# Kernel tuning notes

Hardware: AMD Instinct MI355X
Metric: run time of the kernel (lower is better)

The kernel has to match this reference:

```python
import jax, jax.numpy as jnp
import numpy as np

B, T, C = 2, 4096, 2048
N = 64
H = C // N
D_W, D_A, D_MV, D_G = 96, 96, 64, 256
LN_EPS = 0.00064


def setup_inputs() -> dict:
    key = jax.random.key(0)
    ks = jax.random.split(key, 32)
    rn = lambda k, shape, s=1.0: jax.random.normal(k, shape, jnp.float32) * s
    inp = {}
    inp["x"] = rn(ks[0], (B, T, C))
    inp["v_first"] = rn(ks[1], (B, T, C))
    # token-shift mixing coefficients (in (0,1) like 1 - ddd**p)
    for i, name in enumerate(["x_r", "x_w", "x_k", "x_v", "x_a", "x_g"]):
        inp[name] = jax.random.uniform(ks[2 + i], (1, 1, C), jnp.float32)
    # decay LoRA: w0 in roughly [-6, -0.5]
    inp["w0"] = jax.random.uniform(ks[8], (1, 1, C), jnp.float32, -6.0, -0.5)
    inp["w1"] = rn(ks[9], (C, D_W), 0.05)
    inp["w2"] = rn(ks[10], (D_W, C), 0.05)
    # in-context-learning-rate (a) LoRA
    inp["a0"] = rn(ks[11], (1, 1, C), 0.3) - 0.19
    inp["a1"] = rn(ks[12], (C, D_A), 0.05)
    inp["a2"] = rn(ks[13], (D_A, C), 0.05)
    # value-mix LoRA (layer_id > 0)
    inp["v0"] = rn(ks[14], (1, 1, C), 0.2) + 0.73
    inp["v1"] = rn(ks[15], (C, D_MV), 0.05)
    inp["v2"] = rn(ks[16], (D_MV, C), 0.05)
    # gate LoRA
    inp["g1"] = rn(ks[17], (C, D_G), 0.05)
    inp["g2"] = rn(ks[18], (D_G, C), 0.05)
    inp["k_k"] = rn(ks[19], (1, 1, C), 0.05) + 0.71
    inp["k_a"] = rn(ks[20], (1, 1, C), 0.02) + 1.02
    inp["r_k"] = rn(ks[21], (H, N), 0.02) - 0.04
    sc = 0.5 / C ** 0.5
    inp["W_r"] = jax.random.uniform(ks[22], (C, C), jnp.float32, -sc, sc)
    inp["W_k"] = jax.random.uniform(ks[23], (C, C), jnp.float32, -0.1 * sc, 0.1 * sc)
    inp["W_v"] = jax.random.uniform(ks[24], (C, C), jnp.float32, -sc, sc)
    inp["W_o"] = rn(ks[25], (C, C), 0.02)
    inp["ln_w"] = jnp.ones((C,), jnp.float32)
    inp["ln_b"] = jnp.zeros((C,), jnp.float32)
    return inp


def _wkv7(r, wdec, k, v, a, b):
    # r,wdec,k,v,a,b: [B,T,C]; per-head delta-rule scan, state S: [B,H,Nv,Nk]
    def heads(t):
        return t.reshape(B, T, H, N).transpose(1, 0, 2, 3)  # [T,B,H,N]

    def step(S, ins):
        r_t, w_t, k_t, v_t, a_t, b_t = ins  # each [B,H,N]
        sa = jnp.einsum('bhvk,bhk->bhv', S, a_t)
        S = (S * w_t[:, :, None, :]
             + sa[..., None] * b_t[:, :, None, :]
             + v_t[..., None] * k_t[:, :, None, :])
        y_t = jnp.einsum('bhvk,bhk->bhv', S, r_t)
        return S, y_t

    S0 = jnp.zeros((B, H, N, N), r.dtype)
    _, ys = jax.lax.scan(step, S0, (heads(r), heads(wdec), heads(k), heads(v), heads(a), heads(b)))
    return ys.transpose(1, 0, 2, 3).reshape(B, T, C)


def reference(x, v_first, x_r, x_w, x_k, x_v, x_a, x_g,
              w0, w1, w2, a0, a1, a2, v0, v1, v2, g1, g2,
              k_k, k_a, r_k, W_r, W_k, W_v, W_o, ln_w, ln_b):
    # token shift: prepend zero row, drop last
    xx = jnp.concatenate([jnp.zeros_like(x[:, :1]), x[:, :-1]], axis=1) - x
    xr = x + xx * x_r
    xw = x + xx * x_w
    xk = x + xx * x_k
    xv = x + xx * x_v
    xa = x + xx * x_a
    xg = x + xx * x_g
    r = xr @ W_r.T
    k = xk @ W_k.T
    v = xv @ W_v.T
    w = -jax.nn.softplus(-(w0 + jnp.tanh(xw @ w1) @ w2)) - 0.5
    # layer_id > 0: mix with first-layer value
    v = v + (v_first - v) * jax.nn.sigmoid(v0 + xv @ v1 @ v2)
    a = jax.nn.sigmoid(a0 + xa @ a1 @ a2)
    g = jax.nn.sigmoid(xg @ g1) @ g2
    kk = k * k_k
    kkh = kk.reshape(B, T, H, N)
    kkh = kkh / jnp.maximum(jnp.linalg.norm(kkh, axis=-1, keepdims=True), 1e-12)
    kk = kkh.reshape(B, T, C)
    k = k * (1.0 + (a - 1.0) * k_a)
    wdec = jnp.exp(-jnp.exp(w))  # RWKV7 decay parameterization
    y = _wkv7(r, wdec, k, v, -kk, kk * a)
    # GroupNorm(H groups) over channels per token
    yh = y.reshape(B, T, H, N)
    mu = yh.mean(-1, keepdims=True)
    var = yh.var(-1, keepdims=True)
    y = ((yh - mu) / jnp.sqrt(var + LN_EPS)).reshape(B, T, C) * ln_w + ln_b
    # bonus term
    rh, kh, vh = (t.reshape(B, T, H, N) for t in (r, k, v))
    bonus = ((rh * kh * r_k).sum(-1, keepdims=True) * vh).reshape(B, T, C)
    y = y + bonus
    return (y * g) @ W_o.T
```

## Files before the change

kernel.cpp:

```cpp
#include <hip/hip_runtime.h>
#include <hip/hip_bf16.h>
#include <stdint.h>
#include <math.h>

#define DEV __device__ __forceinline__

typedef __hip_bfloat16 bf16;
typedef __attribute__((ext_vector_type(8))) __bf16 bf16x8;
typedef __attribute__((ext_vector_type(4))) float f32x4;
typedef __attribute__((ext_vector_type(2))) float f32x2;

static constexpr int B_ = 2;
static constexpr int T_ = 4096;
static constexpr int C_ = 2048;
static constexpr int H_ = 32;

DEV void gld_lds16(const void* g, void* l) {
  __builtin_amdgcn_global_load_lds((const __attribute__((address_space(1))) void*)g,
                                   (__attribute__((address_space(3))) void*)l, 16, 0, 0);
}
DEV float bfbits2f(unsigned short u) {
  unsigned int x = ((unsigned int)u) << 16;
  return __builtin_bit_cast(float, x);
}
DEV unsigned short f2bfbits(float f) { bf16 h = __float2bfloat16(f); return __builtin_bit_cast(unsigned short, h); }
DEV void store_bf16x4(bf16* p, f32x4 v) {
  ushort4 u;
  u.x = f2bfbits(v.x); u.y = f2bfbits(v.y); u.z = f2bfbits(v.z); u.w = f2bfbits(v.w);
  *reinterpret_cast<ushort4*>(p) = u;
}
DEV float wsum64(float v) {
#pragma unroll
  for (int m = 32; m > 0; m >>= 1) v += __shfl_xor(v, m, 64);
  return v;
}
template<int CTRL>
DEV float dpp_add(float v) {
  int x = __builtin_bit_cast(int, v);
  int y = __builtin_amdgcn_update_dpp(0, x, CTRL, 0xf, 0xf, false);
  return v + __builtin_bit_cast(float, y);
}
DEV float red16(float v) {
  v = dpp_add<0xB1>(v);
  v = dpp_add<0x4E>(v);
  v = dpp_add<0x124>(v);
  v = dpp_add<0x128>(v);
  return v;
}
DEV f32x4 cvt4(uint2 u) {
  f32x4 o;
  o.x = __builtin_bit_cast(float, u.x << 16);
  o.y = __builtin_bit_cast(float, u.x & 0xFFFF0000u);
  o.z = __builtin_bit_cast(float, u.y << 16);
  o.w = __builtin_bit_cast(float, u.y & 0xFFFF0000u);
  return o;
}

template<int MODE>
__global__ __launch_bounds__(256)
void gemm_bt(const bf16* __restrict__ A, const bf16* __restrict__ Bm,
             void* __restrict__ Cout, const float* __restrict__ ep,
             int N, int K, int T4)
{
  __shared__ bf16 lA[128 * 64];
  __shared__ bf16 lB[128 * 64];
  const int tid  = threadIdx.x;
  const int wave = tid >> 6;
  const int lane = tid & 63;
  const long brow = (long)blockIdx.x * 128;
  const long bcol = (long)blockIdx.y * 128;
  const int wr = wave >> 1, wc = wave & 1;

  f32x4 acc[4][4];
#pragma unroll
  for (int m = 0; m < 4; ++m)
#pragma unroll
    for (int n = 0; n < 4; ++n)
      acc[m][n] = f32x4{0.f, 0.f, 0.f, 0.f};

  const bf16* pa = A  + (size_t)(brow + wave * 32 + (lane >> 3)) * K + (lane & 7) * 8;
  const bf16* pb = Bm + (size_t)(bcol + wave * 32 + (lane >> 3)) * K + (lane & 7) * 8;

  for (int k0 = 0; k0 < K; k0 += 64) {
#pragma unroll
    for (int i = 0; i < 4; ++i) gld_lds16(pa + (size_t)i * 8 * K, &lA[(wave * 4 + i) * 512]);
#pragma unroll
    for (int i = 0; i < 4; ++i) gld_lds16(pb + (size_t)i * 8 * K, &lB[(wave * 4 + i) * 512]);
    pa += 64; pb += 64;
    __syncthreads();
#pragma unroll
    for (int kk = 0; kk < 2; ++kk) {
      bf16x8 af[4], bfv[4];
#pragma unroll
      for (int m = 0; m < 4; ++m)
        af[m] = *(const bf16x8*)&lA[(wr * 64 + m * 16 + (lane & 15)) * 64 + kk * 32 + (lane >> 4) * 8];
#pragma unroll
      for (int n = 0; n < 4; ++n)
        bfv[n] = *(const bf16x8*)&lB[(wc * 64 + n * 16 + (lane & 15)) * 64 + kk * 32 + (lane >> 4) * 8];
#pragma unroll
      for (int m = 0; m < 4; ++m)
#pragma unroll
        for (int n = 0; n < 4; ++n)
          acc[m][n] = __builtin_amdgcn_mfma_f32_16x16x32_bf16(af[m], bfv[n], acc[m][n], 0, 0, 0);
    }
    __syncthreads();
  }

  const int cr = (lane >> 4) * 4;
  const int cc = lane & 15;
#pragma unroll
  for (int m = 0; m < 4; ++m) {
#pragma unroll
    for (int n = 0; n < 4; ++n) {
#pragma unroll
      for (int j = 0; j < 4; ++j) {
        long gm = brow + wr * 64 + m * 16 + cr + j;
        long gn = bcol + wc * 64 + n * 16 + cc;
        float val = acc[m][n][j];
        if constexpr (MODE == 0) {
          ((float*)Cout)[gm * N + gn] = val;
        } else if constexpr (MODE == 2) {
          ((bf16*)Cout)[gm * N + gn] = __float2bfloat16(val);
        } else if constexpr (MODE == 3) {
          ((bf16*)Cout)[gm * N + gn] = __float2bfloat16(tanhf(val));
        } else if constexpr (MODE == 4) {
          ((bf16*)Cout)[gm * N + gn] = __float2bfloat16(1.f / (1.f + expf(-val)));
        } else if constexpr (MODE == 7) {
          long b = gm / T4, t = gm % T4;
          ((bf16*)Cout)[((b * (N >> 6) + (gn >> 6)) * T4 + t) * 64 + (gn & 63)] = __float2bfloat16(val);
        } else if constexpr (MODE == 8) {
          float u = ep[gn] + val;
          float w = -log1pf(expf(-u)) - 0.5f;
          float wd = expf(-expf(w));
          long b = gm / T4, t = gm % T4;
          ((float*)Cout)[((b * (N >> 6) + (gn >> 6)) * T4 + t) * 64 + (gn & 63)] = wd;
        } else if constexpr (MODE == 9) {
          float sg = 1.f / (1.f + expf(-(ep[gn] + val)));
          long b = gm / T4, t = gm % T4;
          ((bf16*)Cout)[((b * (N >> 6) + (gn >> 6)) * T4 + t) * 64 + (gn & 63)] = __float2bfloat16(sg);
        }
      }
    }
  }
}

__global__ __launch_bounds__(256)
void mix1(const float* __restrict__ x, const float* __restrict__ coef,
          bf16* __restrict__ out)
{
  size_t e = ((size_t)blockIdx.x * 256 + threadIdx.x) * 4;
  int c = (int)(e & (C_ - 1));
  size_t m = e >> 11;
  f32x4 xc = *(const f32x4*)(x + e);
  f32x4 xp;
  if ((m & (T_ - 1)) == 0) xp = f32x4{0.f, 0.f, 0.f, 0.f};
  else                     xp = *(const f32x4*)(x + e - C_);
  f32x4 cf = *(const f32x4*)(coef + c);
  store_bf16x4(out + e, xc + (xp - xc) * cf);
}

__global__ __launch_bounds__(256)
void cvt1(const float* __restrict__ s, bf16* __restrict__ d)
{
  size_t e = ((size_t)blockIdx.x * 256 + threadIdx.x) * 4;
  store_bf16x4(d + e, *(const f32x4*)(s + e));
}

struct TPJob { const float* s; bf16* d; int R, Cs, NP, RP; };
struct TP8 { TPJob j[8]; };
__global__ __launch_bounds__(256)
void tpad(TP8 jobs)
{
  TPJob J = jobs.j[blockIdx.y];
  int i = blockIdx.x * 256 + threadIdx.x;
  int tot = J.NP * J.RP;
  if (i >= tot) return;
  int n = i / J.RP, r = i - n * J.RP;
  float v = (n < J.Cs && r < J.R) ? J.s[(size_t)r * J.Cs + n] : 0.f;
  J.d[i] = __float2bfloat16(v);
}

__global__ __launch_bounds__(256)
void prescan2(const bf16* __restrict__ r16, bf16* __restrict__ k16,
              bf16* __restrict__ v16, bf16* __restrict__ ab,
              bf16* __restrict__ vn16,
              const float* __restrict__ vfirst, const float* __restrict__ kkc,
              const float* __restrict__ kac, const float* __restrict__ rk,
              float* __restrict__ sbonus)
{
  const int wid = threadIdx.x >> 6;
  const int lane = threadIdx.x & 63;
  const long id = (long)blockIdx.x * 4 + wid;
  const long bh = id >> 12;
  const long t = id & (T_ - 1);
  const long b = bh >> 5, h = bh & (H_ - 1);
  const long mrow = b * T_ + t;
  const int c = (int)(h * 64 + lane);
  const size_t tp = (size_t)id * 64 + lane;
  float k  = __bfloat162float(k16[tp]);
  float v  = __bfloat162float(v16[tp]);
  float r  = __bfloat162float(r16[tp]);
  float a  = __bfloat162float(ab[tp]);
  float vs = __bfloat162float(vn16[tp]);
  float vf = vfirst[mrow * C_ + c];
  float kkv = k * kkc[c];
  float ssum = wsum64(kkv * kkv);
  float kkn = kkv / fmaxf(sqrtf(ssum), 1e-12f);
  float kn = k * (1.f + (a - 1.f) * kac[c]);
  float vn = v + (vf - v) * vs;
  k16[tp] = __float2bfloat16(kn);
  v16[tp] = __float2bfloat16(vn);
  ab[tp]  = __float2bfloat16(kkn * a);
  vn16[tp] = __float2bfloat16(kkn);
  float bs = wsum64(r * kn * rk[c]);
  if (lane == 0) sbonus[id] = bs;
}

struct SS {
  uint2 r0, r1, k0, k1, n0, n1, b0, b1;
  f32x4 w0, w1;
  unsigned short v0, v1;
};
DEV SS ldss(const uint2* pr, const uint2* pk, const uint2* pn, const uint2* pb,
            const f32x4* pw, const unsigned short* pv, int ss, int kq, int row)
{
  SS s;
  int i0 = ss * 32 + kq, i1 = i0 + 16;
  s.r0 = pr[i0]; s.r1 = pr[i1];
  s.k0 = pk[i0]; s.k1 = pk[i1];
  s.n0 = pn[i0]; s.n1 = pn[i1];
  s.b0 = pb[i0]; s.b1 = pb[i1];
  s.w0 = pw[i0]; s.w1 = pw[i1];
  int j0 = ss * 128 + row, j1 = j0 + 64;
  s.v0 = pv[j0]; s.v1 = pv[j1];
  return s;
}
DEV float dostep(f32x4& S, uint2 ru, uint2 ku, uint2 nu, uint2 bu,
                 f32x4 W, unsigned short vus)
{
  f32x4 R = cvt4(ru), K = cvt4(ku), N = cvt4(nu), Bv = cvt4(bu);
  float vt = bfbits2f(vus);
  f32x2 acc = S.xy * N.xy;
  acc = __builtin_elementwise_fma(S.zw, N.zw, acc);
  float sa = red16(acc.x + acc.y);
  float nsa = -sa;
  f32x2 ns2 = f32x2{nsa, nsa}, vt2 = f32x2{vt, vt};
  S.xy = __builtin_elementwise_fma(vt2, K.xy,
           __builtin_elementwise_fma(ns2, Bv.xy, S.xy * W.xy));
  S.zw = __builtin_elementwise_fma(vt2, K.zw,
           __builtin_elementwise_fma(ns2, Bv.zw, S.zw * W.zw));
  f32x2 yq = S.xy * R.xy;
  yq = __builtin_elementwise_fma(S.zw, R.zw, yq);
  return red16(yq.x + yq.y);
}
DEV void consume(f32x4& S, const SS& s, bf16* py, int t, int kq)
{
  float y0 = dostep(S, s.r0, s.k0, s.n0, s.b0, s.w0, s.v0);
  if (kq == 0) py[(size_t)t * 64] = __float2bfloat16(y0);
  float y1 = dostep(S, s.r1, s.k1, s.n1, s.b1, s.w1, s.v1);
  if (kq == 0) py[(size_t)(t + 1) * 64] = __float2bfloat16(y1);
}
__global__ __launch_bounds__(256, 1)
void wkv_scan5(const bf16* __restrict__ r16, const float* __restrict__ w32,
               const bf16* __restrict__ k16, const bf16* __restrict__ v16,
               const bf16* __restrict__ n16, const bf16* __restrict__ b16,
               bf16* __restrict__ y16)
{
  const int bh = blockIdx.x & 63;
  const int quarter = blockIdx.x >> 6;
  const int wv = threadIdx.x >> 6;
  const int lane = threadIdx.x & 63;
  const int vl = lane >> 4;
  const int kq = lane & 15;
  const int row = quarter * 16 + wv * 4 + vl;
  const size_t eb = (size_t)bh * (T_ * 64);
  const uint2* pr = (const uint2*)(r16 + eb);
  const uint2* pk = (const uint2*)(k16 + eb);
  const uint2* pn = (const uint2*)(n16 + eb);
  const uint2* pb = (const uint2*)(b16 + eb);
  const f32x4* pw = (const f32x4*)(w32 + eb);
  const unsigned short* pv = (const unsigned short*)(v16 + eb);
  bf16* py = y16 + eb + row;

  f32x4 S = f32x4{0.f, 0.f, 0.f, 0.f};
  const int NS = T_ / 2;

  SS s0 = ldss(pr, pk, pn, pb, pw, pv, 0, kq, row);
  SS s1 = ldss(pr, pk, pn, pb, pw, pv, 1, kq, row);
  SS s2 = ldss(pr, pk, pn, pb, pw, pv, 2, kq, row);
  SS s3 = ldss(pr, pk, pn, pb, pw, pv, 3, kq, row);

  for (int ss = 0; ss < NS; ss += 4) {
    int n0 = ss + 4 < NS ? ss + 4 : NS - 1;
    int n1 = ss + 5 < NS ? ss + 5 : NS - 1;
    int n2 = ss + 6 < NS ? ss + 6 : NS - 1;
    int n3 = ss + 7 < NS ? ss + 7 : NS - 1;
    SS p0 = ldss(pr, pk, pn, pb, pw, pv, n0, kq, row);
    consume(S, s0, py, 2 * ss, kq);
    SS p1 = ldss(pr, pk, pn, pb, pw, pv, n1, kq, row);
    consume(S, s1, py, 2 * ss + 2, kq);
    SS p2 = ldss(pr, pk, pn, pb, pw, pv, n2, kq, row);
    consume(S, s2, py, 2 * ss + 4, kq);
    SS p3 = ldss(pr, pk, pn, pb, pw, pv, n3, kq, row);
    consume(S, s3, py, 2 * ss + 6, kq);
    s0 = p0; s1 = p1; s2 = p2; s3 = p3;
  }
}

__global__ __launch_bounds__(256)
void postk2(const bf16* __restrict__ y16, const bf16* __restrict__ v16,
            const float* __restrict__ sbonus, const bf16* __restrict__ g16,
            const float* __restrict__ lnw, const float* __restrict__ lnb,
            bf16* __restrict__ opre)
{
  const int wid = threadIdx.x >> 6;
  const int lane = threadIdx.x & 63;
  const long id = (long)blockIdx.x * 4 + wid;
  const long bh = id >> 12;
  const long t = id & (T_ - 1);
  const long b = bh >> 5, h = bh & (H_ - 1);
  const long mrow = b * T_ + t;
  const int c = (int)(h * 64 + lane);
  const size_t tp = (size_t)id * 64 + lane;
  float y = __bfloat162float(y16[tp]);
  float mu = wsum64(y) * (1.f / 64.f);
  float d = y - mu;
  float var = wsum64(d * d) * (1.f / 64.f);
  float yn = d * rsqrtf(var + 0.00064f) * lnw[c] + lnb[c];
  float outv = (yn + sbonus[id] * __bfloat162float(v16[tp]))
               * __bfloat162float(g16[mrow * C_ + c]);
  opre[mrow * C_ + c] = __float2bfloat16(outv);
}

extern "C" void kernel_launch(void* const* d_in, const int* in_sizes, int n_in,
                              void* d_out, int out_size, void* d_ws, size_t ws_size,
                              hipStream_t stream)
{
  const float* x    = (const float*)d_in[0];
  const float* vfst = (const float*)d_in[1];
  const float* x_r  = (const float*)d_in[2];
  const float* x_w  = (const float*)d_in[3];
  const float* x_k  = (const float*)d_in[4];
  const float* x_v  = (const float*)d_in[5];
  const float* x_a  = (const float*)d_in[6];
  const float* x_g  = (const float*)d_in[7];
  const float* w0   = (const float*)d_in[8];
  const float* w1   = (const float*)d_in[9];
  const float* w2   = (const float*)d_in[10];
  const float* a0   = (const float*)d_in[11];
  const float* a1   = (const float*)d_in[12];
  const float* a2   = (const float*)d_in[13];
  const float* v0   = (const float*)d_in[14];
  const float* v1   = (const float*)d_in[15];
  const float* v2   = (const float*)d_in[16];
  const float* g1   = (const float*)d_in[17];
  const float* g2   = (const float*)d_in[18];
  const float* k_k  = (const float*)d_in[19];
  const float* k_a  = (const float*)d_in[20];
  const float* r_k  = (const float*)d_in[21];
  const float* W_r  = (const float*)d_in[22];
  const float* W_k  = (const float*)d_in[23];
  const float* W_v  = (const float*)d_in[24];
  const float* W_o  = (const float*)d_in[25];
  const float* lnw  = (const float*)d_in[26];
  const float* lnb  = (const float*)d_in[27];

  const size_t MB = 1048576ULL;
  const size_t HK = 524288ULL;
  if (ws_size < 248 * MB) return;

  char* ws = (char*)d_ws;
  bf16* r16  = (bf16*)(ws + 0 * MB);
  bf16* k16  = (bf16*)(ws + 32 * MB);
  bf16* v16  = (bf16*)(ws + 64 * MB);
  float* w32 = (float*)(ws + 96 * MB);
  bf16* opre = (bf16*)(ws + 96 * MB);
  bf16* asig = (bf16*)(ws + 160 * MB);
  bf16* vsig = (bf16*)(ws + 192 * MB);
  bf16* w1t = (bf16*)(ws + 224 * MB);
  bf16* a1t = (bf16*)(ws + 224 * MB + HK);
  bf16* v1t = (bf16*)(ws + 225 * MB);
  bf16* g1t = (bf16*)(ws + 225 * MB + HK);
  bf16* w2t = (bf16*)(ws + 226 * MB + HK);
  bf16* a2t = (bf16*)(ws + 227 * MB);
  bf16* v2t = (bf16*)(ws + 227 * MB + HK);
  bf16* g2t = (bf16*)(ws + 228 * MB);
  bf16* h_w = (bf16*)(ws + 229 * MB);
  bf16* h_a = (bf16*)(ws + 231 * MB);
  bf16* h_v = (bf16*)(ws + 233 * MB);
  bf16* h_g = (bf16*)(ws + 235 * MB);
  float* sb = (float*)(ws + 239 * MB);
  bf16* WB  = (bf16*)(ws + 240 * MB);
  bf16* g16 = (bf16*)d_out;
  bf16* MIX = (bf16*)((char*)d_out + 32 * MB);
  bf16* y16 = (bf16*)((char*)d_out + 32 * MB);

  TP8 jobs;
  jobs.j[0] = TPJob{ w1, w1t, 2048,   96,  128, 2048 };
  jobs.j[1] = TPJob{ a1, a1t, 2048,   96,  128, 2048 };
  jobs.j[2] = TPJob{ v1, v1t, 2048,   64,  128, 2048 };
  jobs.j[3] = TPJob{ g1, g1t, 2048,  256,  256, 2048 };
  jobs.j[4] = TPJob{ w2, w2t,   96, 2048, 2048,  128 };
  jobs.j[5] = TPJob{ a2, a2t,   96, 2048, 2048,  128 };
  jobs.j[6] = TPJob{ v2, v2t,   64, 2048, 2048,  128 };
  jobs.j[7] = TPJob{ g2, g2t,  256, 2048, 2048,  256 };
  tpad<<<dim3(2048, 8), 256, 0, stream>>>(jobs);

  mix1<<<dim3(16384), 256, 0, stream>>>(x, x_w, MIX);
  gemm_bt<3><<<dim3(64, 1), 256, 0, stream>>>(MIX, w1t, h_w, nullptr, 128, 2048, 0);
  mix1<<<dim3(16384), 256, 0, stream>>>(x, x_a, MIX);
  gemm_bt<2><<<dim3(64, 1), 256, 0, stream>>>(MIX, a1t, h_a, nullptr, 128, 2048, 0);
  mix1<<<dim3(16384), 256, 0, stream>>>(x, x_v, MIX);
  gemm_bt<2><<<dim3(64, 1), 256, 0, stream>>>(MIX, v1t, h_v, nullptr, 128, 2048, 0);
  mix1<<<dim3(16384), 256, 0, stream>>>(x, x_g, MIX);
  gemm_bt<4><<<dim3(64, 2), 256, 0, stream>>>(MIX, g1t, h_g, nullptr, 256, 2048, 0);

  gemm_bt<8><<<dim3(64, 16), 256, 0, stream>>>(h_w, w2t, w32, w0, 2048, 128, T_);
  gemm_bt<9><<<dim3(64, 16), 256, 0, stream>>>(h_a, a2t, asig, a0, 2048, 128, T_);
  gemm_bt<9><<<dim3(64, 16), 256, 0, stream>>>(h_v, v2t, vsig, v0, 2048, 128, T_);
  gemm_bt<2><<<dim3(64, 16), 256, 0, stream>>>(h_g, g2t, g16, nullptr, 2048, 256, 0);

  cvt1<<<dim3(4096), 256, 0, stream>>>(W_r, WB);
  mix1<<<dim3(16384), 256, 0, stream>>>(x, x_r, MIX);
  gemm_bt<7><<<dim3(64, 16), 256, 0, stream>>>(MIX, WB, r16, nullptr, 2048, 2048, T_);
  cvt1<<<dim3(4096), 256, 0, stream>>>(W_k, WB);
  mix1<<<dim3(16384), 256, 0, stream>>>(x, x_k, MIX);
  gemm_bt<7><<<dim3(64, 16), 256, 0, stream>>>(MIX, WB, k16, nullptr, 2048, 2048, T_);
  cvt1<<<dim3(4096), 256, 0, stream>>>(W_v, WB);
  mix1<<<dim3(16384), 256, 0, stream>>>(x, x_v, MIX);
  gemm_bt<7><<<dim3(64, 16), 256, 0, stream>>>(MIX, WB, v16, nullptr, 2048, 2048, T_);

  prescan2<<<dim3(65536), 256, 0, stream>>>(r16, k16, v16, asig, vsig,
                                            vfst, k_k, k_a, r_k, sb);
  wkv_scan5<<<dim3(256), 256, 0, stream>>>(r16, w32, k16, v16, vsig, asig, y16);
  postk2<<<dim3(65536), 256, 0, stream>>>(y16, v16, sb, g16, lnw, lnb, opre);

  cvt1<<<dim3(4096), 256, 0, stream>>>(W_o, WB);
  gemm_bt<0><<<dim3(64, 16), 256, 0, stream>>>(opre, WB, (float*)d_out, nullptr, 2048, 2048, 0);
}
```

Baseline: 1.952 ms.

## Split WKV scan state across 32 lanes per row and double block count

The recurrent WKV scan now gives each state row to 32 lanes holding 2 state elements each, instead of 16 lanes holding 4. The grid doubles from 256 to 512 blocks and launch bounds allow two blocks per CU, which should put more waves on the latency-bound serial scan. The price is an extra cross-row shuffle in every reduction and more total load instructions for the same data.

Result: slower. 2.136 ms (+9.4%).

```diff
diff --git a/kernel.cpp b/kernel.cpp
--- a/kernel.cpp
+++ b/kernel.cpp
@@ -18,10 +18,6 @@
 DEV void gld_lds16(const void* g, void* l) {
   __builtin_amdgcn_global_load_lds((const __attribute__((address_space(1))) void*)g,
                                    (__attribute__((address_space(3))) void*)l, 16, 0, 0);
-}
-DEV float bfbits2f(unsigned short u) {
-  unsigned int x = ((unsigned int)u) << 16;
-  return __builtin_bit_cast(float, x);
 }
 DEV unsigned short f2bfbits(float f) { bf16 h = __float2bfloat16(f); return __builtin_bit_cast(unsigned short, h); }
 DEV void store_bf16x4(bf16* p, f32x4 v) {
@@ -29,6 +25,10 @@
   u.x = f2bfbits(v.x); u.y = f2bfbits(v.y); u.z = f2bfbits(v.z); u.w = f2bfbits(v.w);
   *reinterpret_cast<ushort4*>(p) = u;
 }
+DEV float bfbits2f(unsigned short u) {
+  unsigned int x = ((unsigned int)u) << 16;
+  return __builtin_bit_cast(float, x);
+}
 DEV float wsum64(float v) {
 #pragma unroll
   for (int m = 32; m > 0; m >>= 1) v += __shfl_xor(v, m, 64);
@@ -40,19 +40,18 @@
   int y = __builtin_amdgcn_update_dpp(0, x, CTRL, 0xf, 0xf, false);
   return v + __builtin_bit_cast(float, y);
 }
-DEV float red16(float v) {
+DEV float red32(float v) {
   v = dpp_add<0xB1>(v);
   v = dpp_add<0x4E>(v);
   v = dpp_add<0x124>(v);
   v = dpp_add<0x128>(v);
+  v += __shfl_xor(v, 16, 64);
   return v;
 }
-DEV f32x4 cvt4(uint2 u) {
-  f32x4 o;
-  o.x = __builtin_bit_cast(float, u.x << 16);
-  o.y = __builtin_bit_cast(float, u.x & 0xFFFF0000u);
-  o.z = __builtin_bit_cast(float, u.y << 16);
-  o.w = __builtin_bit_cast(float, u.y & 0xFFFF0000u);
+DEV f32x2 cvt2(unsigned int u) {
+  f32x2 o;
+  o.x = __builtin_bit_cast(float, u << 16);
+  o.y = __builtin_bit_cast(float, u & 0xFFFF0000u);
   return o;
 }
 
@@ -216,93 +215,90 @@
   if (lane == 0) sbonus[id] = bs;
 }
 
-struct SS {
-  uint2 r0, r1, k0, k1, n0, n1, b0, b1;
-  f32x4 w0, w1;
+struct SS2 {
+  unsigned int r0, r1, k0, k1, n0, n1, b0, b1;
+  f32x2 w0, w1;
   unsigned short v0, v1;
 };
-DEV SS ldss(const uint2* pr, const uint2* pk, const uint2* pn, const uint2* pb,
-            const f32x4* pw, const unsigned short* pv, int ss, int kq, int row)
-{
-  SS s;
-  int i0 = ss * 32 + kq, i1 = i0 + 16;
+DEV SS2 ldss2(const unsigned int* pr, const unsigned int* pk,
+              const unsigned int* pn, const unsigned int* pb,
+              const f32x2* pw, const unsigned short* pv, int ss, int kq, int row)
+{
+  SS2 s;
+  int i0 = ss * 64 + kq, i1 = i0 + 32;
   s.r0 = pr[i0]; s.r1 = pr[i1];
   s.k0 = pk[i0]; s.k1 = pk[i1];
   s.n0 = pn[i0]; s.n1 = pn[i1];
   s.b0 = pb[i0]; s.b1 = pb[i1];
   s.w0 = pw[i0]; s.w1 = pw[i1];
-  int j0 = ss * 128 + row, j1 = j0 + 64;
-  s.v0 = pv[j0]; s.v1 = pv[j1];
+  int j0 = ss * 128 + row;
+  s.v0 = pv[j0]; s.v1 = pv[j0 + 64];
   return s;
 }
-DEV float dostep(f32x4& S, uint2 ru, uint2 ku, uint2 nu, uint2 bu,
-                 f32x4 W, unsigned short vus)
-{
-  f32x4 R = cvt4(ru), K = cvt4(ku), N = cvt4(nu), Bv = cvt4(bu);
+DEV float dostep2(f32x2& S, unsigned int ru, unsigned int ku, unsigned int nu,
+                  unsigned int bu, f32x2 W, unsigned short vus)
+{
+  f32x2 R = cvt2(ru), K = cvt2(ku), N = cvt2(nu), Bv = cvt2(bu);
   float vt = bfbits2f(vus);
-  f32x2 acc = S.xy * N.xy;
-  acc = __builtin_elementwise_fma(S.zw, N.zw, acc);
-  float sa = red16(acc.x + acc.y);
+  f32x2 t = S * N;
+  float sa = red32(t.x + t.y);
   float nsa = -sa;
   f32x2 ns2 = f32x2{nsa, nsa}, vt2 = f32x2{vt, vt};
-  S.xy = __builtin_elementwise_fma(vt2, K.xy,
-           __builtin_elementwise_fma(ns2, Bv.xy, S.xy * W.xy));
-  S.zw = __builtin_elementwise_fma(vt2, K.zw,
-           __builtin_elementwise_fma(ns2, Bv.zw, S.zw * W.zw));
-  f32x2 yq = S.xy * R.xy;
-  yq = __builtin_elementwise_fma(S.zw, R.zw, yq);
-  return red16(yq.x + yq.y);
-}
-DEV void consume(f32x4& S, const SS& s, bf16* py, int t, int kq)
-{
-  float y0 = dostep(S, s.r0, s.k0, s.n0, s.b0, s.w0, s.v0);
+  S = __builtin_elementwise_fma(vt2, K,
+        __builtin_elementwise_fma(ns2, Bv, S * W));
+  f32x2 yq = S * R;
+  return red32(yq.x + yq.y);
+}
+DEV void consume2(f32x2& S, const SS2& s, bf16* py, int t, int kq)
+{
+  float y0 = dostep2(S, s.r0, s.k0, s.n0, s.b0, s.w0, s.v0);
   if (kq == 0) py[(size_t)t * 64] = __float2bfloat16(y0);
-  float y1 = dostep(S, s.r1, s.k1, s.n1, s.b1, s.w1, s.v1);
+  float y1 = dostep2(S, s.r1, s.k1, s.n1, s.b1, s.w1, s.v1);
   if (kq == 0) py[(size_t)(t + 1) * 64] = __float2bfloat16(y1);
 }
-__global__ __launch_bounds__(256, 1)
-void wkv_scan5(const bf16* __restrict__ r16, const float* __restrict__ w32,
+__global__ __launch_bounds__(256, 2)
+void wkv_scan6(const bf16* __restrict__ r16, const float* __restrict__ w32,
                const bf16* __restrict__ k16, const bf16* __restrict__ v16,
                const bf16* __restrict__ n16, const bf16* __restrict__ b16,
                bf16* __restrict__ y16)
 {
   const int bh = blockIdx.x & 63;
-  const int quarter = blockIdx.x >> 6;
+  const int g = blockIdx.x >> 6;
   const int wv = threadIdx.x >> 6;
   const int lane = threadIdx.x & 63;
-  const int vl = lane >> 4;
-  const int kq = lane & 15;
-  const int row = quarter * 16 + wv * 4 + vl;
+  const int vl = lane >> 5;
+  const int kq = lane & 31;
+  const int row = g * 8 + wv * 2 + vl;
   const size_t eb = (size_t)bh * (T_ * 64);
-  const uint2* pr = (const uint2*)(r16 + eb);
-  const uint2* pk = (const uint2*)(k16 + eb);
-  const uint2* pn = (const uint2*)(n16 + eb);
-  const uint2* pb = (const uint2*)(b16 + eb);
-  const f32x4* pw = (const f32x4*)(w32 + eb);
+  const unsigned int* pr = (const unsigned int*)(r16 + eb);
+  const unsigned int* pk = (const unsigned int*)(k16 + eb);
+  const unsigned int* pn = (const unsigned int*)(n16 + eb);
+  const unsigned int* pb = (const unsigned int*)(b16 + eb);
+  const f32x2* pw = (const f32x2*)(w32 + eb);
   const unsigned short* pv = (const unsigned short*)(v16 + eb);
   bf16* py = y16 + eb + row;
 
-  f32x4 S = f32x4{0.f, 0.f, 0.f, 0.f};
+  f32x2 S = f32x2{0.f, 0.f};
   const int NS = T_ / 2;
 
-  SS s0 = ldss(pr, pk, pn, pb, pw, pv, 0, kq, row);
-  SS s1 = ldss(pr, pk, pn, pb, pw, pv, 1, kq, row);
-  SS s2 = ldss(pr, pk, pn, pb, pw, pv, 2, kq, row);
-  SS s3 = ldss(pr, pk, pn, pb, pw, pv, 3, kq, row);
+  SS2 s0 = ldss2(pr, pk, pn, pb, pw, pv, 0, kq, row);
+  SS2 s1 = ldss2(pr, pk, pn, pb, pw, pv, 1, kq, row);
+  SS2 s2 = ldss2(pr, pk, pn, pb, pw, pv, 2, kq, row);
+  SS2 s3 = ldss2(pr, pk, pn, pb, pw, pv, 3, kq, row);
 
   for (int ss = 0; ss < NS; ss += 4) {
     int n0 = ss + 4 < NS ? ss + 4 : NS - 1;
     int n1 = ss + 5 < NS ? ss + 5 : NS - 1;
     int n2 = ss + 6 < NS ? ss + 6 : NS - 1;
     int n3 = ss + 7 < NS ? ss + 7 : NS - 1;
-    SS p0 = ldss(pr, pk, pn, pb, pw, pv, n0, kq, row);
-    consume(S, s0, py, 2 * ss, kq);
-    SS p1 = ldss(pr, pk, pn, pb, pw, pv, n1, kq, row);
-    consume(S, s1, py, 2 * ss + 2, kq);
-    SS p2 = ldss(pr, pk, pn, pb, pw, pv, n2, kq, row);
-    consume(S, s2, py, 2 * ss + 4, kq);
-    SS p3 = ldss(pr, pk, pn, pb, pw, pv, n3, kq, row);
-    consume(S, s3, py, 2 * ss + 6, kq);
+    SS2 p0 = ldss2(pr, pk, pn, pb, pw, pv, n0, kq, row);
+    consume2(S, s0, py, 2 * ss, kq);
+    SS2 p1 = ldss2(pr, pk, pn, pb, pw, pv, n1, kq, row);
+    consume2(S, s1, py, 2 * ss + 2, kq);
+    SS2 p2 = ldss2(pr, pk, pn, pb, pw, pv, n2, kq, row);
+    consume2(S, s2, py, 2 * ss + 4, kq);
+    SS2 p3 = ldss2(pr, pk, pn, pb, pw, pv, n3, kq, row);
+    consume2(S, s3, py, 2 * ss + 6, kq);
     s0 = p0; s1 = p1; s2 = p2; s3 = p3;
   }
 }
@@ -432,7 +428,7 @@
 
   prescan2<<<dim3(65536), 256, 0, stream>>>(r16, k16, v16, asig, vsig,
                                             vfst, k_k, k_a, r_k, sb);
-  wkv_scan5<<<dim3(256), 256, 0, stream>>>(r16, w32, k16, v16, vsig, asig, y16);
+  wkv_scan6<<<dim3(512), 256, 0, stream>>>(r16, w32, k16, v16, vsig, asig, y16);
   postk2<<<dim3(65536), 256, 0, stream>>>(y16, v16, sb, g16, lnw, lnb, opre);
 
   cvt1<<<dim3(4096), 256, 0, stream>>>(W_o, WB);
```

## Batch LoRA GEMMs into multi-job launches, fuse token-shift mixes and weight conversion

Applied to the files above, without the earlier changes.

The four LoRA token-shift mixes are computed in one kernel that reads x once and writes four bf16 buffers. The eight small LoRA GEMMs are grouped into two multi-job launches so their blocks run concurrently instead of as tiny serial grids. Weight conversion is fused with each R/K/V mix into one launch. The scan loop gets sched_barriers to pin load/compute interleaving. The epilogue mode becomes a runtime switch, which costs a little per-store branching, and the new mix buffers reuse workspace regions that are later overwritten.

Result: slower. 2.130 ms (+9.1%).

```diff
diff --git a/kernel.cpp b/kernel.cpp
--- a/kernel.cpp
+++ b/kernel.cpp
@@ -18,16 +18,16 @@
 DEV void gld_lds16(const void* g, void* l) {
   __builtin_amdgcn_global_load_lds((const __attribute__((address_space(1))) void*)g,
                                    (__attribute__((address_space(3))) void*)l, 16, 0, 0);
-}
-DEV float bfbits2f(unsigned short u) {
-  unsigned int x = ((unsigned int)u) << 16;
-  return __builtin_bit_cast(float, x);
 }
 DEV unsigned short f2bfbits(float f) { bf16 h = __float2bfloat16(f); return __builtin_bit_cast(unsigned short, h); }
 DEV void store_bf16x4(bf16* p, f32x4 v) {
   ushort4 u;
   u.x = f2bfbits(v.x); u.y = f2bfbits(v.y); u.z = f2bfbits(v.z); u.w = f2bfbits(v.w);
   *reinterpret_cast<ushort4*>(p) = u;
+}
+DEV float bfbits2f(unsigned short u) {
+  unsigned int x = ((unsigned int)u) << 16;
+  return __builtin_bit_cast(float, x);
 }
 DEV float wsum64(float v) {
 #pragma unroll
@@ -56,19 +56,14 @@
   return o;
 }
 
-template<int MODE>
-__global__ __launch_bounds__(256)
-void gemm_bt(const bf16* __restrict__ A, const bf16* __restrict__ Bm,
-             void* __restrict__ Cout, const float* __restrict__ ep,
-             int N, int K, int T4)
-{
-  __shared__ bf16 lA[128 * 64];
-  __shared__ bf16 lB[128 * 64];
+DEV void gemm_body(const bf16* __restrict__ A, const bf16* __restrict__ Bm,
+                   void* __restrict__ Cout, const float* __restrict__ ep,
+                   int N, int K, long brow, long bcol, int mode,
+                   bf16* lA, bf16* lB)
+{
   const int tid  = threadIdx.x;
   const int wave = tid >> 6;
   const int lane = tid & 63;
-  const long brow = (long)blockIdx.x * 128;
-  const long bcol = (long)blockIdx.y * 128;
   const int wr = wave >> 1, wc = wave & 1;
 
   f32x4 acc[4][4];
@@ -117,46 +112,96 @@
         long gm = brow + wr * 64 + m * 16 + cr + j;
         long gn = bcol + wc * 64 + n * 16 + cc;
         float val = acc[m][n][j];
-        if constexpr (MODE == 0) {
-          ((float*)Cout)[gm * N + gn] = val;
-        } else if constexpr (MODE == 2) {
-          ((bf16*)Cout)[gm * N + gn] = __float2bfloat16(val);
-        } else if constexpr (MODE == 3) {
-          ((bf16*)Cout)[gm * N + gn] = __float2bfloat16(tanhf(val));
-        } else if constexpr (MODE == 4) {
-          ((bf16*)Cout)[gm * N + gn] = __float2bfloat16(1.f / (1.f + expf(-val)));
-        } else if constexpr (MODE == 7) {
-          long b = gm / T4, t = gm % T4;
-          ((bf16*)Cout)[((b * (N >> 6) + (gn >> 6)) * T4 + t) * 64 + (gn & 63)] = __float2bfloat16(val);
-        } else if constexpr (MODE == 8) {
-          float u = ep[gn] + val;
-          float w = -log1pf(expf(-u)) - 0.5f;
-          float wd = expf(-expf(w));
-          long b = gm / T4, t = gm % T4;
-          ((float*)Cout)[((b * (N >> 6) + (gn >> 6)) * T4 + t) * 64 + (gn & 63)] = wd;
-        } else if constexpr (MODE == 9) {
-          float sg = 1.f / (1.f + expf(-(ep[gn] + val)));
-          long b = gm / T4, t = gm % T4;
-          ((bf16*)Cout)[((b * (N >> 6) + (gn >> 6)) * T4 + t) * 64 + (gn & 63)] = __float2bfloat16(sg);
+        switch (mode) {
+          case 0: ((float*)Cout)[gm * N + gn] = val; break;
+          case 2: ((bf16*)Cout)[gm * N + gn] = __float2bfloat16(val); break;
+          case 3: ((bf16*)Cout)[gm * N + gn] = __float2bfloat16(tanhf(val)); break;
+          case 4: ((bf16*)Cout)[gm * N + gn] = __float2bfloat16(1.f / (1.f + expf(-val))); break;
+          case 7: {
+            long b = gm / T_, t = gm % T_;
+            ((bf16*)Cout)[((b * (N >> 6) + (gn >> 6)) * T_ + t) * 64 + (gn & 63)] = __float2bfloat16(val);
+          } break;
+          case 8: {
+            float u = ep[gn] + val;
+            float w = -log1pf(expf(-u)) - 0.5f;
+            float wd = expf(-expf(w));
+            long b = gm / T_, t = gm % T_;
+            ((float*)Cout)[((b * (N >> 6) + (gn >> 6)) * T_ + t) * 64 + (gn & 63)] = wd;
+          } break;
+          case 9: {
+            float sg = 1.f / (1.f + expf(-(ep[gn] + val)));
+            long b = gm / T_, t = gm % T_;
+            ((bf16*)Cout)[((b * (N >> 6) + (gn >> 6)) * T_ + t) * 64 + (gn & 63)] = __float2bfloat16(sg);
+          } break;
         }
       }
     }
   }
 }
 
-__global__ __launch_bounds__(256)
-void mix1(const float* __restrict__ x, const float* __restrict__ coef,
-          bf16* __restrict__ out)
+template<int MODE>
+__global__ __launch_bounds__(256)
+void gemm_bt(const bf16* __restrict__ A, const bf16* __restrict__ Bm,
+             void* __restrict__ Cout, const float* __restrict__ ep,
+             int N, int K, int T4)
+{
+  __shared__ bf16 lA[128 * 64];
+  __shared__ bf16 lB[128 * 64];
+  gemm_body(A, Bm, Cout, ep, N, K, (long)blockIdx.x * 128, (long)blockIdx.y * 128,
+            MODE, lA, lB);
+}
+
+struct GJ { const bf16* A; const bf16* Bm; void* C; const float* ep; int N, K, mode, ytile; };
+struct GJ8 { GJ j[8]; };
+__global__ __launch_bounds__(256)
+void gemm_multi(GJ8 jobs)
+{
+  __shared__ bf16 lA[128 * 64];
+  __shared__ bf16 lB[128 * 64];
+  GJ J = jobs.j[blockIdx.z];
+  gemm_body(J.A, J.Bm, J.C, J.ep, J.N, J.K, (long)blockIdx.x * 128,
+            (long)(blockIdx.y + J.ytile) * 128, J.mode, lA, lB);
+}
+
+__global__ __launch_bounds__(256)
+void mix4k(const float* __restrict__ x,
+           const float* __restrict__ c0, const float* __restrict__ c1,
+           const float* __restrict__ c2, const float* __restrict__ c3,
+           bf16* __restrict__ o0, bf16* __restrict__ o1,
+           bf16* __restrict__ o2, bf16* __restrict__ o3)
 {
   size_t e = ((size_t)blockIdx.x * 256 + threadIdx.x) * 4;
   int c = (int)(e & (C_ - 1));
   size_t m = e >> 11;
   f32x4 xc = *(const f32x4*)(x + e);
-  f32x4 xp;
-  if ((m & (T_ - 1)) == 0) xp = f32x4{0.f, 0.f, 0.f, 0.f};
-  else                     xp = *(const f32x4*)(x + e - C_);
-  f32x4 cf = *(const f32x4*)(coef + c);
-  store_bf16x4(out + e, xc + (xp - xc) * cf);
+  f32x4 dx;
+  if ((m & (T_ - 1)) == 0) dx = f32x4{0.f, 0.f, 0.f, 0.f} - xc;
+  else                     dx = *(const f32x4*)(x + e - C_) - xc;
+  store_bf16x4(o0 + e, xc + dx * (*(const f32x4*)(c0 + c)));
+  store_bf16x4(o1 + e, xc + dx * (*(const f32x4*)(c1 + c)));
+  store_bf16x4(o2 + e, xc + dx * (*(const f32x4*)(c2 + c)));
+  store_bf16x4(o3 + e, xc + dx * (*(const f32x4*)(c3 + c)));
+}
+
+__global__ __launch_bounds__(256)
+void cvtmix(const float* __restrict__ W, bf16* __restrict__ WB,
+            const float* __restrict__ x, const float* __restrict__ coef,
+            bf16* __restrict__ MIX)
+{
+  if (blockIdx.x < 4096) {
+    size_t e = ((size_t)blockIdx.x * 256 + threadIdx.x) * 4;
+    store_bf16x4(WB + e, *(const f32x4*)(W + e));
+  } else {
+    size_t e = ((size_t)(blockIdx.x - 4096) * 256 + threadIdx.x) * 4;
+    int c = (int)(e & (C_ - 1));
+    size_t m = e >> 11;
+    f32x4 xc = *(const f32x4*)(x + e);
+    f32x4 xp;
+    if ((m & (T_ - 1)) == 0) xp = f32x4{0.f, 0.f, 0.f, 0.f};
+    else                     xp = *(const f32x4*)(x + e - C_);
+    f32x4 cf = *(const f32x4*)(coef + c);
+    store_bf16x4(MIX + e, xc + (xp - xc) * cf);
+  }
 }
 
 __global__ __launch_bounds__(256)
@@ -231,8 +276,8 @@
   s.n0 = pn[i0]; s.n1 = pn[i1];
   s.b0 = pb[i0]; s.b1 = pb[i1];
   s.w0 = pw[i0]; s.w1 = pw[i1];
-  int j0 = ss * 128 + row, j1 = j0 + 64;
-  s.v0 = pv[j0]; s.v1 = pv[j1];
+  int j0 = ss * 128 + row;
+  s.v0 = pv[j0]; s.v1 = pv[j0 + 64];
   return s;
 }
 DEV float dostep(f32x4& S, uint2 ru, uint2 ku, uint2 nu, uint2 bu,
@@ -261,7 +306,7 @@
   if (kq == 0) py[(size_t)(t + 1) * 64] = __float2bfloat16(y1);
 }
 __global__ __launch_bounds__(256, 1)
-void wkv_scan5(const bf16* __restrict__ r16, const float* __restrict__ w32,
+void wkv_scan7(const bf16* __restrict__ r16, const float* __restrict__ w32,
                const bf16* __restrict__ k16, const bf16* __restrict__ v16,
                const bf16* __restrict__ n16, const bf16* __restrict__ b16,
                bf16* __restrict__ y16)
@@ -289,6 +334,7 @@
   SS s1 = ldss(pr, pk, pn, pb, pw, pv, 1, kq, row);
   SS s2 = ldss(pr, pk, pn, pb, pw, pv, 2, kq, row);
   SS s3 = ldss(pr, pk, pn, pb, pw, pv, 3, kq, row);
+  __builtin_amdgcn_sched_barrier(0);
 
   for (int ss = 0; ss < NS; ss += 4) {
     int n0 = ss + 4 < NS ? ss + 4 : NS - 1;
@@ -296,12 +342,16 @@
     int n2 = ss + 6 < NS ? ss + 6 : NS - 1;
     int n3 = ss + 7 < NS ? ss + 7 : NS - 1;
     SS p0 = ldss(pr, pk, pn, pb, pw, pv, n0, kq, row);
+    __builtin_amdgcn_sched_barrier(0);
     consume(S, s0, py, 2 * ss, kq);
     SS p1 = ldss(pr, pk, pn, pb, pw, pv, n1, kq, row);
+    __builtin_amdgcn_sched_barrier(0);
     consume(S, s1, py, 2 * ss + 2, kq);
     SS p2 = ldss(pr, pk, pn, pb, pw, pv, n2, kq, row);
+    __builtin_amdgcn_sched_barrier(0);
     consume(S, s2, py, 2 * ss + 4, kq);
     SS p3 = ldss(pr, pk, pn, pb, pw, pv, n3, kq, row);
+    __builtin_amdgcn_sched_barrier(0);
     consume(S, s3, py, 2 * ss + 6, kq);
     s0 = p0; s1 = p1; s2 = p2; s3 = p3;
   }
@@ -370,6 +420,10 @@
   if (ws_size < 248 * MB) return;
 
   char* ws = (char*)d_ws;
+  bf16* xw = (bf16*)(ws + 0 * MB);
+  bf16* xa = (bf16*)(ws + 32 * MB);
+  bf16* xv = (bf16*)(ws + 64 * MB);
+  bf16* xg = (bf16*)(ws + 96 * MB);
   bf16* r16  = (bf16*)(ws + 0 * MB);
   bf16* k16  = (bf16*)(ws + 32 * MB);
   bf16* v16  = (bf16*)(ws + 64 * MB);
@@ -406,33 +460,33 @@
   jobs.j[7] = TPJob{ g2, g2t,  256, 2048, 2048,  256 };
   tpad<<<dim3(2048, 8), 256, 0, stream>>>(jobs);
 
-  mix1<<<dim3(16384), 256, 0, stream>>>(x, x_w, MIX);
-  gemm_bt<3><<<dim3(64, 1), 256, 0, stream>>>(MIX, w1t, h_w, nullptr, 128, 2048, 0);
-  mix1<<<dim3(16384), 256, 0, stream>>>(x, x_a, MIX);
-  gemm_bt<2><<<dim3(64, 1), 256, 0, stream>>>(MIX, a1t, h_a, nullptr, 128, 2048, 0);
-  mix1<<<dim3(16384), 256, 0, stream>>>(x, x_v, MIX);
-  gemm_bt<2><<<dim3(64, 1), 256, 0, stream>>>(MIX, v1t, h_v, nullptr, 128, 2048, 0);
-  mix1<<<dim3(16384), 256, 0, stream>>>(x, x_g, MIX);
-  gemm_bt<4><<<dim3(64, 2), 256, 0, stream>>>(MIX, g1t, h_g, nullptr, 256, 2048, 0);
-
-  gemm_bt<8><<<dim3(64, 16), 256, 0, stream>>>(h_w, w2t, w32, w0, 2048, 128, T_);
-  gemm_bt<9><<<dim3(64, 16), 256, 0, stream>>>(h_a, a2t, asig, a0, 2048, 128, T_);
-  gemm_bt<9><<<dim3(64, 16), 256, 0, stream>>>(h_v, v2t, vsig, v0, 2048, 128, T_);
-  gemm_bt<2><<<dim3(64, 16), 256, 0, stream>>>(h_g, g2t, g16, nullptr, 2048, 256, 0);
-
-  cvt1<<<dim3(4096), 256, 0, stream>>>(W_r, WB);
-  mix1<<<dim3(16384), 256, 0, stream>>>(x, x_r, MIX);
+  mix4k<<<dim3(16384), 256, 0, stream>>>(x, x_w, x_a, x_v, x_g, xw, xa, xv, xg);
+
+  GJ8 s1j = {};
+  s1j.j[0] = GJ{ xw, w1t, h_w, nullptr, 128, 2048, 3, 0 };
+  s1j.j[1] = GJ{ xa, a1t, h_a, nullptr, 128, 2048, 2, 0 };
+  s1j.j[2] = GJ{ xv, v1t, h_v, nullptr, 128, 2048, 2, 0 };
+  s1j.j[3] = GJ{ xg, g1t, h_g, nullptr, 256, 2048, 4, 0 };
+  s1j.j[4] = GJ{ xg, g1t, h_g, nullptr, 256, 2048, 4, 1 };
+  gemm_multi<<<dim3(64, 1, 5), 256, 0, stream>>>(s1j);
+
+  GJ8 s2j = {};
+  s2j.j[0] = GJ{ h_w, w2t, w32,  w0,      2048, 128, 8, 0 };
+  s2j.j[1] = GJ{ h_a, a2t, asig, a0,      2048, 128, 9, 0 };
+  s2j.j[2] = GJ{ h_v, v2t, vsig, v0,      2048, 128, 9, 0 };
+  s2j.j[3] = GJ{ h_g, g2t, g16,  nullptr, 2048, 256, 2, 0 };
+  gemm_multi<<<dim3(64, 16, 4), 256, 0, stream>>>(s2j);
+
+  cvtmix<<<dim3(20480), 256, 0, stream>>>(W_r, WB, x, x_r, MIX);
   gemm_bt<7><<<dim3(64, 16), 256, 0, stream>>>(MIX, WB, r16, nullptr, 2048, 2048, T_);
-  cvt1<<<dim3(4096), 256, 0, stream>>>(W_k, WB);
-  mix1<<<dim3(16384), 256, 0, stream>>>(x, x_k, MIX);
+  cvtmix<<<dim3(20480), 256, 0, stream>>>(W_k, WB, x, x_k, MIX);
   gemm_bt<7><<<dim3(64, 16), 256, 0, stream>>>(MIX, WB, k16, nullptr, 2048, 2048, T_);
-  cvt1<<<dim3(4096), 256, 0, stream>>>(W_v, WB);
-  mix1<<<dim3(16384), 256, 0, stream>>>(x, x_v, MIX);
+  cvtmix<<<dim3(20480), 256, 0, stream>>>(W_v, WB, x, x_v, MIX);
   gemm_bt<7><<<dim3(64, 16), 256, 0, stream>>>(MIX, WB, v16, nullptr, 2048, 2048, T_);
 
   prescan2<<<dim3(65536), 256, 0, stream>>>(r16, k16, v16, asig, vsig,
                                             vfst, k_k, k_a, r_k, sb);
-  wkv_scan5<<<dim3(256), 256, 0, stream>>>(r16, w32, k16, v16, vsig, asig, y16);
+  wkv_scan7<<<dim3(256), 256, 0, stream>>>(r16, w32, k16, v16, vsig, asig, y16);
   postk2<<<dim3(65536), 256, 0, stream>>>(y16, v16, sb, g16, lnw, lnb, opre);
 
   cvt1<<<dim3(4096), 256, 0, stream>>>(W_o, WB);
```
